# Kernel tuning notes

Hardware: AMD Instinct MI355X
Metric: run time of the kernel (lower is better)

Reference implementation:

```python
import jax, jax.numpy as jnp
import numpy as np

P = 512        # number of graph pairs
MAXN = 192     # max(len_s) by construction
D_IN = 32      # num_input_features
HID = 64       # hidden_dim
REG = 0.1      # entropic reg
ITERS = 8      # numItermax in forward call
DEG = 8        # avg degree for synthetic edges


def setup_inputs() -> dict:
    key = jax.random.key(0)
    ks = jax.random.split(key, 16)
    len_s = np.asarray(96 + (np.arange(P) % 97), dtype=np.int32)          # 96..192
    len_t = np.asarray(32 + ((np.arange(P) * 7) % 65), dtype=np.int32)    # 32..96 <= len_s
    Ns, Nt = int(len_s.sum()), int(len_t.sum())
    return {
        "x_s": jax.random.normal(ks[0], (Ns, D_IN), jnp.float32),
        "x_t": jax.random.normal(ks[1], (Nt, D_IN), jnp.float32),
        "W_rel0": 0.1 * jax.random.normal(ks[2], (D_IN, HID), jnp.float32),
        "b_rel0": 0.1 * jax.random.normal(ks[3], (HID,), jnp.float32),
        "W_root0": 0.1 * jax.random.normal(ks[4], (D_IN, HID), jnp.float32),
        "W_rel1": 0.1 * jax.random.normal(ks[5], (HID, HID), jnp.float32),
        "b_rel1": 0.1 * jax.random.normal(ks[6], (HID,), jnp.float32),
        "W_root1": 0.1 * jax.random.normal(ks[7], (HID, HID), jnp.float32),
        "W_e": 0.1 * jax.random.normal(ks[8], (D_IN + 2 * HID, 64), jnp.float32),
        "b_e": 0.1 * jax.random.normal(ks[9], (64,), jnp.float32),
        "virtual": jax.random.uniform(ks[10], (64,), jnp.float32),
        "edge_index_s": jax.random.randint(ks[11], (2, Ns * DEG), 0, Ns, dtype=jnp.int32),
        "edge_index_t": jax.random.randint(ks[12], (2, Nt * DEG), 0, Nt, dtype=jnp.int32),
        "len_s": jnp.asarray(len_s),
        "len_t": jnp.asarray(len_t),
    }


def _normalize(x):
    return x / jnp.clip(jnp.linalg.norm(x, axis=-1, keepdims=True), 1e-12)


def _gnn_embed(x, ei, layers, W_e, b_e):
    # GraphConv: out = lin_rel(sum_{j->i} x_j) + lin_root(x_i), then relu; cat all layer outputs
    outs = [x]
    h = x
    for (Wr, br, Wo) in layers:
        agg = jax.ops.segment_sum(h[ei[0]], ei[1], num_segments=h.shape[0])
        h = jax.nn.relu(agg @ Wr + br + h @ Wo)
        outs.append(h)
    emb = jnp.concatenate(outs, axis=1) @ W_e + b_e
    return _normalize(emb)


def _pad_gather(emb, lens):
    # [total, E] -> [P, MAXN, E] via per-pair offsets (indices clipped; invalid masked later)
    off = jnp.cumsum(lens) - lens
    idx = jnp.clip(off[:, None] + jnp.arange(MAXN)[None, :], 0, emb.shape[0] - 1)
    return emb[idx]


def reference(x_s, x_t, W_rel0, b_rel0, W_root0, W_rel1, b_rel1, W_root1,
              W_e, b_e, virtual, edge_index_s, edge_index_t, len_s, len_t):
    layers = [(W_rel0, b_rel0, W_root0), (W_rel1, b_rel1, W_root1)]
    emb_s = _gnn_embed(x_s, edge_index_s, layers, W_e, b_e)  # [Ns, 64]
    emb_t = _gnn_embed(x_t, edge_index_t, layers, W_e, b_e)  # [Nt, 64]
    virt = _normalize(virtual[None, :])[0]

    s_pad = _pad_gather(emb_s, len_s)  # [P, MAXN, 64]
    t_pad = _pad_gather(emb_t, len_t)  # [P, MAXN, 64]
    j = jnp.arange(MAXN)
    # columns >= len_t use the virtual node embedding (covers j in [m, n))
    t_mask = (j[None, :] < len_t[:, None])[:, :, None]
    t_aug = jnp.where(t_mask, t_pad, virt[None, None, :])

    # Euclidean cdist via quadratic expansion
    sq_s = jnp.sum(s_pad * s_pad, -1)                              # [P, MAXN]
    sq_t = jnp.sum(t_aug * t_aug, -1)                              # [P, MAXN]
    dot = jnp.einsum('pid,pjd->pij', s_pad, t_aug)                 # [P, MAXN, MAXN]
    cd = jnp.sqrt(jnp.maximum(sq_s[:, :, None] + sq_t[:, None, :] - 2.0 * dot, 1e-12))

    # padded cost: real block = cdist, bottom-right pad block = 0, rest = 1000
    row_valid = j[None, :] < len_s[:, None]                        # [P, MAXN] (n = len_s)
    in_block = row_valid[:, :, None] & row_valid[:, None, :]
    pad_block = (~row_valid)[:, :, None] & (~row_valid)[:, None, :]
    cost = jnp.where(in_block, cd, jnp.where(pad_block, 0.0, 1000.0))

    # Sinkhorn-Knopp, a = b = ones(MAXN) so Kp = K and updates are 1/(K v), 1/(K^T u)
    K = jnp.exp(-cost / REG)

    def body(_, uv):
        u, v = uv
        v = 1.0 / jnp.einsum('pij,pi->pj', K, u)
        u = 1.0 / jnp.einsum('pij,pj->pi', K, v)
        return (u, v)

    u0 = jnp.full((P, MAXN), 1.0 / MAXN, dtype=cost.dtype)
    u, v = jax.lax.fori_loop(0, ITERS, body, (u0, u0))
    gamma = jax.lax.stop_gradient(u[:, :, None] * K * v[:, None, :])

    geds = jnp.sum(gamma * cost, axis=(1, 2))
    geds2 = geds / (len_s + len_t).astype(cost.dtype)
    return gamma, cost, geds2
```

## Files before the change

kernel.cpp:

```cpp
#include <hip/hip_runtime.h>
#include <math.h>

#define PAIRS 512
#define MAXN 192

__global__ void offsets_kernel(const int* __restrict__ ls, const int* __restrict__ lt,
                               int* __restrict__ off) {
    __shared__ int wa[8], wb[8];
    int t = threadIdx.x;
    int a = ls[t], b = lt[t];
    int ia = a, ib = b;
#pragma unroll
    for (int d = 1; d < 64; d <<= 1) {
        int xa = __shfl_up(ia, d, 64);
        int xb = __shfl_up(ib, d, 64);
        if ((t & 63) >= d) { ia += xa; ib += xb; }
    }
    if ((t & 63) == 63) { wa[t >> 6] = ia; wb[t >> 6] = ib; }
    __syncthreads();
    int pa = 0, pb = 0;
    for (int w = 0; w < (t >> 6); w++) { pa += wa[w]; pb += wb[w]; }
    off[t] = pa + ia - a;
    off[PAIRS + t] = pb + ib - b;
}

__global__ __launch_bounds__(256) void count2_kernel(const int* __restrict__ eiS,
                                                     const int* __restrict__ eiT,
                                                     int* __restrict__ cnt,
                                                     int Es, int Et, int split) {
    int e = blockIdx.x * 256 + threadIdx.x;
    if (e < Es) atomicAdd(&cnt[eiS[Es + e]], 1);
    else if (e < Es + Et) atomicAdd(&cnt[split + eiT[Et + (e - Es)]], 1);
}

__global__ __launch_bounds__(256) void scan1_kernel(int* __restrict__ data,
                                                    int* __restrict__ blockSums, int N) {
    __shared__ int sc[256];
    int t = threadIdx.x;
    int base = blockIdx.x * 1024;
    int v[4];
    int s = 0;
#pragma unroll
    for (int q = 0; q < 4; q++) {
        int i = base + t * 4 + q;
        v[q] = (i < N) ? data[i] : 0;
        s += v[q];
    }
    sc[t] = s;
    __syncthreads();
    for (int d = 1; d < 256; d <<= 1) {
        int x = (t >= d) ? sc[t - d] : 0;
        __syncthreads();
        sc[t] += x;
        __syncthreads();
    }
    int excl = sc[t] - s;
#pragma unroll
    for (int q = 0; q < 4; q++) {
        int i = base + t * 4 + q;
        if (i < N) { data[i] = excl; excl += v[q]; }
    }
    if (t == 255) blockSums[blockIdx.x] = sc[255];
}

__global__ void scan2_kernel(int* __restrict__ blockSums, int B) {
    __shared__ int sh[256];
    int t = threadIdx.x;
    int v = (t < B) ? blockSums[t] : 0;
    sh[t] = v;
    __syncthreads();
    for (int d = 1; d < 256; d <<= 1) {
        int x = (t >= d) ? sh[t - d] : 0;
        __syncthreads();
        sh[t] += x;
        __syncthreads();
    }
    if (t < B) blockSums[t] = sh[t] - v;
}

__global__ __launch_bounds__(256) void scan3_kernel(int* __restrict__ data,
                                                    const int* __restrict__ blockSums,
                                                    int* __restrict__ cursor, int N) {
    int i = blockIdx.x * 256 + threadIdx.x;
    if (i < N) {
        int v = data[i] + blockSums[i >> 10];
        data[i] = v;
        cursor[i] = v;
    }
}

__global__ __launch_bounds__(256) void fill2_kernel(const int* __restrict__ eiS,
                                                    const int* __restrict__ eiT,
                                                    int* __restrict__ cursor,
                                                    int* __restrict__ src,
                                                    int Es, int Et, int split) {
    int e = blockIdx.x * 256 + threadIdx.x;
    if (e < Es) {
        int p = atomicAdd(&cursor[eiS[Es + e]], 1);
        src[p] = eiS[e];
    } else if (e < Es + Et) {
        int ee = e - Es;
        int p = atomicAdd(&cursor[split + eiT[Et + ee]], 1);
        src[p] = eiT[ee];
    }
}

template <int F>
__global__ __launch_bounds__(256) void gather_kernel(const float* __restrict__ featA,
                                                     const float* __restrict__ featB,
                                                     int split,
                                                     const int* __restrict__ rs,
                                                     const int* __restrict__ re,
                                                     const int* __restrict__ src,
                                                     float* __restrict__ agg, int N) {
    int gid = blockIdx.x * 256 + threadIdx.x;
    int row = gid / F;
    int lane = threadIdx.x & (F - 1);
    if (row >= N) return;
    int b = rs[row], e = re[row];
    int cnt = e - b;
    const float* feat = (row < split) ? featA : featB;
    int pre = cnt < F ? cnt : F;
    int sidx = (lane < cnt) ? src[b + lane] : 0;
    float acc = 0.f;
    for (int q = 0; q < pre; q++) {
        int s = __shfl(sidx, q, F);
        acc += feat[(size_t)s * F + lane];
    }
    for (int q = b + F; q < e; q++) acc += feat[(size_t)src[q] * F + lane];
    agg[(size_t)row * F + lane] = acc;
}


template <int KIN>
__global__ __launch_bounds__(256) void lin_gemm_kernel(const float* __restrict__ agg,
    const float* __restrict__ hinA, const float* __restrict__ hinB, int split,
    const float* __restrict__ Wrel, const float* __restrict__ brel,
    const float* __restrict__ Wroot, float* __restrict__ hout, int N) {
    __shared__ float Abuf[64 * 65];
    __shared__ float4 Wbuf[64 * 16];
    int tid = threadIdx.x;
    int i = tid & 15, j = tid >> 4;
    int rowbase = blockIdx.x * 64;
    float4 bv = ((const float4*)brel)[j];
    float acc[4][4];
#pragma unroll
    for (int r = 0; r < 4; r++) { acc[r][0] = bv.x; acc[r][1] = bv.y; acc[r][2] = bv.z; acc[r][3] = bv.w; }

    for (int c0 = 0; c0 < 2 * KIN; c0 += 64) {
        __syncthreads();
        for (int t = tid; t < 1024; t += 256) {
            int r = t >> 4, k4 = t & 15;
            int kg = c0 + 4 * k4;
            int row = rowbase + r; if (row >= N) row = N - 1;
            float4 v;
            if (kg < KIN) {
                v = ((const float4*)(agg + (size_t)row * KIN))[kg >> 2];
            } else {
                int kk = kg - KIN;
                const float* h = (row < split) ? hinA + (size_t)row * KIN
                                               : hinB + (size_t)(row - split) * KIN;
                v = ((const float4*)h)[kk >> 2];
            }
            float* d = Abuf + r * 65 + 4 * k4;
            d[0] = v.x; d[1] = v.y; d[2] = v.z; d[3] = v.w;
        }
        for (int t = tid; t < 1024; t += 256) {
            int k = t >> 4, jj = t & 15;
            int kg = c0 + k;
            const float* Wsrc = (kg < KIN) ? (Wrel + (size_t)kg * 64)
                                           : (Wroot + (size_t)(kg - KIN) * 64);
            Wbuf[t] = ((const float4*)Wsrc)[jj];
        }
        __syncthreads();
#pragma unroll 4
        for (int k = 0; k < 64; k++) {
            float4 wv = Wbuf[k * 16 + j];
            float a0 = Abuf[(4 * i + 0) * 65 + k];
            float a1 = Abuf[(4 * i + 1) * 65 + k];
            float a2 = Abuf[(4 * i + 2) * 65 + k];
            float a3 = Abuf[(4 * i + 3) * 65 + k];
            acc[0][0] = fmaf(a0, wv.x, acc[0][0]); acc[0][1] = fmaf(a0, wv.y, acc[0][1]);
            acc[0][2] = fmaf(a0, wv.z, acc[0][2]); acc[0][3] = fmaf(a0, wv.w, acc[0][3]);
            acc[1][0] = fmaf(a1, wv.x, acc[1][0]); acc[1][1] = fmaf(a1, wv.y, acc[1][1]);
            acc[1][2] = fmaf(a1, wv.z, acc[1][2]); acc[1][3] = fmaf(a1, wv.w, acc[1][3]);
            acc[2][0] = fmaf(a2, wv.x, acc[2][0]); acc[2][1] = fmaf(a2, wv.y, acc[2][1]);
            acc[2][2] = fmaf(a2, wv.z, acc[2][2]); acc[2][3] = fmaf(a2, wv.w, acc[2][3]);
            acc[3][0] = fmaf(a3, wv.x, acc[3][0]); acc[3][1] = fmaf(a3, wv.y, acc[3][1]);
            acc[3][2] = fmaf(a3, wv.z, acc[3][2]); acc[3][3] = fmaf(a3, wv.w, acc[3][3]);
        }
    }
#pragma unroll
    for (int r = 0; r < 4; r++) {
        int row = rowbase + 4 * i + r;
        if (row < N) {
            float4 o = make_float4(fmaxf(acc[r][0], 0.f), fmaxf(acc[r][1], 0.f),
                                   fmaxf(acc[r][2], 0.f), fmaxf(acc[r][3], 0.f));
            ((float4*)(hout + (size_t)row * 64))[j] = o;
        }
    }
}

__global__ __launch_bounds__(256) void emb_gemm_kernel(const float* __restrict__ xA,
    const float* __restrict__ xB, int split,
    const float* __restrict__ h1, const float* __restrict__ h2,
    const float* __restrict__ We, const float* __restrict__ be,
    float* __restrict__ emb, int N) {
    __shared__ float Abuf[64 * 65];
    __shared__ float4 Wbuf[64 * 16];
    int tid = threadIdx.x;
    int i = tid & 15, j = tid >> 4;
    int rowbase = blockIdx.x * 64;
    float4 bv = ((const float4*)be)[j];
    float acc[4][4];
#pragma unroll
    for (int r = 0; r < 4; r++) { acc[r][0] = bv.x; acc[r][1] = bv.y; acc[r][2] = bv.z; acc[r][3] = bv.w; }

    for (int c0 = 0; c0 < 160; c0 += 64) {
        int kw = (160 - c0 < 64) ? (160 - c0) : 64;
        int sh = (kw == 64) ? 4 : 3;
        int msk = (1 << sh) - 1;
        __syncthreads();
        for (int t = tid; t < 64 * (kw >> 2); t += 256) {
            int r = t >> sh, k4 = t & msk;
            int kg = c0 + 4 * k4;
            int row = rowbase + r; if (row >= N) row = N - 1;
            float4 v;
            if (kg < 32) {
                const float* x = (row < split) ? xA + (size_t)row * 32
                                               : xB + (size_t)(row - split) * 32;
                v = ((const float4*)x)[kg >> 2];
            } else if (kg < 96) {
                v = ((const float4*)(h1 + (size_t)row * 64))[(kg - 32) >> 2];
            } else {
                v = ((const float4*)(h2 + (size_t)row * 64))[(kg - 96) >> 2];
            }
            float* d = Abuf + r * 65 + 4 * k4;
            d[0] = v.x; d[1] = v.y; d[2] = v.z; d[3] = v.w;
        }
        for (int t = tid; t < kw * 16; t += 256) {
            int k = t >> 4, jj = t & 15;
            Wbuf[t] = ((const float4*)(We + (size_t)(c0 + k) * 64))[jj];
        }
        __syncthreads();
#pragma unroll 4
        for (int k = 0; k < kw; k++) {
            float4 wv = Wbuf[k * 16 + j];
            float a0 = Abuf[(4 * i + 0) * 65 + k];
            float a1 = Abuf[(4 * i + 1) * 65 + k];
            float a2 = Abuf[(4 * i + 2) * 65 + k];
            float a3 = Abuf[(4 * i + 3) * 65 + k];
            acc[0][0] = fmaf(a0, wv.x, acc[0][0]); acc[0][1] = fmaf(a0, wv.y, acc[0][1]);
            acc[0][2] = fmaf(a0, wv.z, acc[0][2]); acc[0][3] = fmaf(a0, wv.w, acc[0][3]);
            acc[1][0] = fmaf(a1, wv.x, acc[1][0]); acc[1][1] = fmaf(a1, wv.y, acc[1][1]);
            acc[1][2] = fmaf(a1, wv.z, acc[1][2]); acc[1][3] = fmaf(a1, wv.w, acc[1][3]);
            acc[2][0] = fmaf(a2, wv.x, acc[2][0]); acc[2][1] = fmaf(a2, wv.y, acc[2][1]);
            acc[2][2] = fmaf(a2, wv.z, acc[2][2]); acc[2][3] = fmaf(a2, wv.w, acc[2][3]);
            acc[3][0] = fmaf(a3, wv.x, acc[3][0]); acc[3][1] = fmaf(a3, wv.y, acc[3][1]);
            acc[3][2] = fmaf(a3, wv.z, acc[3][2]); acc[3][3] = fmaf(a3, wv.w, acc[3][3]);
        }
    }
    __syncthreads();
#pragma unroll
    for (int r = 0; r < 4; r++)
#pragma unroll
        for (int c = 0; c < 4; c++)
            Abuf[(4 * i + r) * 65 + 4 * j + c] = acc[r][c];
    __syncthreads();
    int lane = tid & 63, wv = tid >> 6;
    for (int rr = 0; rr < 16; rr++) {
        int r = wv * 16 + rr;
        float val = Abuf[r * 65 + lane];
        float ss = val * val;
#pragma unroll
        for (int d = 32; d > 0; d >>= 1) ss += __shfl_xor(ss, d, 64);
        int row = rowbase + r;
        if (row < N) emb[(size_t)row * 64 + lane] = val / fmaxf(sqrtf(ss), 1e-12f);
    }
}

__global__ __launch_bounds__(512, 4) void fused_cost_sinkhorn_kernel(
    const float* __restrict__ embS, const float* __restrict__ embT,
    const float* __restrict__ vraw,
    const int* __restrict__ lenS, const int* __restrict__ lenT,
    const int* __restrict__ off,
    float* __restrict__ cost_out, float* __restrict__ gamma_out,
    float* __restrict__ geds2, int Ns) {
    __shared__ __align__(16) float sT[192 * 68];
    __shared__ __align__(16) float sS[96 * 68];
    __shared__ __align__(16) float sqT[192];
    __shared__ __align__(16) float sqS[96];
    __shared__ __align__(16) float virtv[64];

    int p = blockIdx.x;
    int tid = threadIdx.x;
    int ti = tid & 31;
    int tj = tid >> 5;
    int n = lenS[p], m = lenT[p];
    int offs = off[p], offt = off[PAIRS + p];

    if (tid < 64) {
        float v = vraw[tid];
        float ss = v * v;
#pragma unroll
        for (int d = 32; d > 0; d >>= 1) ss += __shfl_xor(ss, d, 64);
        virtv[tid] = v / fmaxf(sqrtf(ss), 1e-12f);
    }
    __syncthreads();

    for (int t = tid; t < 192 * 16; t += 512) {
        int j = t >> 4, q = t & 15;
        float4 vv = (j < m) ? ((const float4*)embT)[(size_t)(offt + j) * 16 + q]
                            : ((const float4*)virtv)[q];
        *(float4*)(sT + j * 68 + 4 * q) = vv;
    }
    __syncthreads();
    if (tid < 192) {
        float s = 0.f;
#pragma unroll
        for (int k = 0; k < 64; k++) { float a = sT[tid * 68 + k]; s = fmaf(a, a, s); }
        sqT[tid] = s;
    }

    float kf[2][3][12];

#pragma unroll
    for (int h = 0; h < 2; h++) {
        __syncthreads();
        for (int t = tid; t < 96 * 16; t += 512) {
            int r = t >> 4, q = t & 15;
            int gi = offs + 96 * h + r;
            if (gi > Ns - 1) gi = Ns - 1;
            float4 vv = ((const float4*)embS)[(size_t)gi * 16 + q];
            *(float4*)(sS + r * 68 + 4 * q) = vv;
        }
        __syncthreads();
        if (tid < 96) {
            float s = 0.f;
#pragma unroll
            for (int k = 0; k < 64; k++) { float a = sS[tid * 68 + k]; s = fmaf(a, a, s); }
            sqS[tid] = s;
        }
        __syncthreads();

#pragma unroll
        for (int s = 0; s < 3; s++)
#pragma unroll
            for (int b = 0; b < 12; b++) kf[h][s][b] = 0.f;

        for (int k4 = 0; k4 < 16; k4++) {
            float4 a0 = *(const float4*)(sS + (3 * ti + 0) * 68 + 4 * k4);
            float4 a1 = *(const float4*)(sS + (3 * ti + 1) * 68 + 4 * k4);
            float4 a2 = *(const float4*)(sS + (3 * ti + 2) * 68 + 4 * k4);
#pragma unroll
            for (int b = 0; b < 12; b++) {
                float4 tb = *(const float4*)(sT + (12 * tj + b) * 68 + 4 * k4);
                kf[h][0][b] = fmaf(a0.x, tb.x, kf[h][0][b]);
                kf[h][0][b] = fmaf(a0.y, tb.y, kf[h][0][b]);
                kf[h][0][b] = fmaf(a0.z, tb.z, kf[h][0][b]);
                kf[h][0][b] = fmaf(a0.w, tb.w, kf[h][0][b]);
                kf[h][1][b] = fmaf(a1.x, tb.x, kf[h][1][b]);
                kf[h][1][b] = fmaf(a1.y, tb.y, kf[h][1][b]);
                kf[h][1][b] = fmaf(a1.z, tb.z, kf[h][1][b]);
                kf[h][1][b] = fmaf(a1.w, tb.w, kf[h][1][b]);
                kf[h][2][b] = fmaf(a2.x, tb.x, kf[h][2][b]);
                kf[h][2][b] = fmaf(a2.y, tb.y, kf[h][2][b]);
                kf[h][2][b] = fmaf(a2.z, tb.z, kf[h][2][b]);
                kf[h][2][b] = fmaf(a2.w, tb.w, kf[h][2][b]);
            }
        }
#pragma unroll
        for (int s = 0; s < 3; s++) {
            int i = 96 * h + 3 * ti + s;
            bool rv = i < n;
            float sqi = sqS[3 * ti + s];
            float tmp[12];
#pragma unroll
            for (int b = 0; b < 12; b++) {
                int j = 12 * tj + b;
                float cd = sqrtf(fmaxf(sqi + sqT[j] - 2.f * kf[h][s][b], 1e-12f));
                float c = (rv && (j < n)) ? cd : ((!rv && (j >= n)) ? 0.f : 1000.f);
                tmp[b] = c;
                kf[h][s][b] = expf(-10.f * c);
            }
            float* orow = cost_out + ((size_t)p * MAXN + i) * MAXN + 12 * tj;
#pragma unroll
            for (int q = 0; q < 3; q++)
                ((float4*)orow)[q] = make_float4(tmp[4 * q], tmp[4 * q + 1],
                                                 tmp[4 * q + 2], tmp[4 * q + 3]);
        }
    }
    __syncthreads();

    float* part = sS;
    float* ubuf = sS + 6336;
    float* vbuf = sqT;

    if (tid < 192) ubuf[tid] = 1.f / 192.f;
    __syncthreads();

    for (int it = 0; it < 8; it++) {
        float uloc[6];
#pragma unroll
        for (int h = 0; h < 2; h++)
#pragma unroll
            for (int s = 0; s < 3; s++) uloc[3 * h + s] = ubuf[96 * h + 3 * ti + s];
#pragma unroll
        for (int b = 0; b < 12; b++) {
            float a = 0.f;
#pragma unroll
            for (int h = 0; h < 2; h++)
#pragma unroll
                for (int s = 0; s < 3; s++) a = fmaf(kf[h][s][b], uloc[3 * h + s], a);
            part[(12 * tj + b) * 33 + ti] = a;
        }
        __syncthreads();
        if (tid < 192) {
            float s = 0.f;
#pragma unroll
            for (int g = 0; g < 32; g++) s += part[tid * 33 + g];
            vbuf[tid] = 1.f / s;
        }
        __syncthreads();
        float vloc[12];
        {
            float4 va = *(const float4*)(vbuf + 12 * tj);
            float4 vb = *(const float4*)(vbuf + 12 * tj + 4);
            float4 vc = *(const float4*)(vbuf + 12 * tj + 8);
            vloc[0] = va.x; vloc[1] = va.y; vloc[2] = va.z; vloc[3] = va.w;
            vloc[4] = vb.x; vloc[5] = vb.y; vloc[6] = vb.z; vloc[7] = vb.w;
            vloc[8] = vc.x; vloc[9] = vc.y; vloc[10] = vc.z; vloc[11] = vc.w;
        }
#pragma unroll
        for (int h = 0; h < 2; h++)
#pragma unroll
            for (int s = 0; s < 3; s++) {
                float a = 0.f;
#pragma unroll
                for (int b = 0; b < 12; b++) a = fmaf(kf[h][s][b], vloc[b], a);
                part[tj * 192 + 96 * h + 3 * ti + s] = a;
            }
        __syncthreads();
        if (tid < 192) {
            float s = 0.f;
#pragma unroll
            for (int g = 0; g < 16; g++) s += part[g * 192 + tid];
            ubuf[tid] = 1.f / s;
        }
        __syncthreads();
    }

    float vloc[12];
    {
        float4 va = *(const float4*)(vbuf + 12 * tj);
        float4 vb = *(const float4*)(vbuf + 12 * tj + 4);
        float4 vc = *(const float4*)(vbuf + 12 * tj + 8);
        vloc[0] = va.x; vloc[1] = va.y; vloc[2] = va.z; vloc[3] = va.w;
        vloc[4] = vb.x; vloc[5] = vb.y; vloc[6] = vb.z; vloc[7] = vb.w;
        vloc[8] = vc.x; vloc[9] = vc.y; vloc[10] = vc.z; vloc[11] = vc.w;
    }
    float accg = 0.f;
#pragma unroll
    for (int h = 0; h < 2; h++)
#pragma unroll
        for (int s = 0; s < 3; s++) {
            int i = 96 * h + 3 * ti + s;
            float ui = ubuf[i];
            float tmp[12];
#pragma unroll
            for (int b = 0; b < 12; b++) {
                float Kij = kf[h][s][b];
                float gg = ui * Kij * vloc[b];
                tmp[b] = gg;
                if (Kij > 0.f) accg = fmaf(gg, -0.1f * logf(Kij), accg);
            }
            float* grow = gamma_out + ((size_t)p * MAXN + i) * MAXN + 12 * tj;
#pragma unroll
            for (int q = 0; q < 3; q++)
                ((float4*)grow)[q] = make_float4(tmp[4 * q], tmp[4 * q + 1],
                                                 tmp[4 * q + 2], tmp[4 * q + 3]);
        }
#pragma unroll
    for (int d = 32; d > 0; d >>= 1) accg += __shfl_xor(accg, d, 64);
    if ((tid & 63) == 0) sqS[tid >> 6] = accg;
    __syncthreads();
    if (tid == 0) {
        float s = 0.f;
        for (int w = 0; w < 8; w++) s += sqS[w];
        geds2[p] = s / (float)(n + m);
    }
}

extern "C" void kernel_launch(void* const* d_in, const int* in_sizes, int n_in,
                              void* d_out, int out_size, void* d_ws, size_t ws_size,
                              hipStream_t stream) {
    const float* x_s     = (const float*)d_in[0];
    const float* x_t     = (const float*)d_in[1];
    const float* W_rel0  = (const float*)d_in[2];
    const float* b_rel0  = (const float*)d_in[3];
    const float* W_root0 = (const float*)d_in[4];
    const float* W_rel1  = (const float*)d_in[5];
    const float* b_rel1  = (const float*)d_in[6];
    const float* W_root1 = (const float*)d_in[7];
    const float* W_e     = (const float*)d_in[8];
    const float* b_e     = (const float*)d_in[9];
    const float* virt    = (const float*)d_in[10];
    const int*   ei_s    = (const int*)d_in[11];
    const int*   ei_t    = (const int*)d_in[12];
    const int*   len_s   = (const int*)d_in[13];
    const int*   len_t   = (const int*)d_in[14];

    int Ns = in_sizes[0] / 32;
    int Nt = in_sizes[1] / 32;
    int Es = in_sizes[11] / 2;
    int Et = in_sizes[12] / 2;
    int Ntot = Ns + Nt;
    int Etot = Es + Et;

    char* w = (char*)d_ws;
    int* off  = (int*)w;              w += 1024 * 4;
    int* bsum = (int*)w;              w += 256 * 4;
    int* rs   = (int*)w;              w += (size_t)Ntot * 4;
    int* cur  = (int*)w;              w += (size_t)Ntot * 4;
    int* src  = (int*)w;              w += (size_t)Etot * 4;
    w = (char*)(((size_t)w + 255) & ~(size_t)255);
    float* agg = (float*)w;           w += (size_t)Ntot * 64 * 4;
    float* h1  = (float*)w;           w += (size_t)Ntot * 64 * 4;
    float* h2  = (float*)w;           w += (size_t)Ntot * 64 * 4;

    float* out_gamma = (float*)d_out;
    float* out_cost  = out_gamma + (size_t)PAIRS * MAXN * MAXN;
    float* out_geds  = out_cost + (size_t)PAIRS * MAXN * MAXN;

    offsets_kernel<<<1, PAIRS, 0, stream>>>(len_s, len_t, off);

    hipMemsetAsync(rs, 0, (size_t)Ntot * 4, stream);
    count2_kernel<<<(Etot + 255) / 256, 256, 0, stream>>>(ei_s, ei_t, rs, Es, Et, Ns);
    int nb = (Ntot + 1023) / 1024;
    scan1_kernel<<<nb, 256, 0, stream>>>(rs, bsum, Ntot);
    scan2_kernel<<<1, 256, 0, stream>>>(bsum, nb);
    scan3_kernel<<<(Ntot + 255) / 256, 256, 0, stream>>>(rs, bsum, cur, Ntot);
    fill2_kernel<<<(Etot + 255) / 256, 256, 0, stream>>>(ei_s, ei_t, cur, src, Es, Et, Ns);

    int gblk = (Ntot + 63) / 64;

    gather_kernel<32><<<(int)(((long long)Ntot * 32 + 255) / 256), 256, 0, stream>>>(
        x_s, x_t, Ns, rs, cur, src, agg, Ntot);
    lin_gemm_kernel<32><<<gblk, 256, 0, stream>>>(
        agg, x_s, x_t, Ns, W_rel0, b_rel0, W_root0, h1, Ntot);
    gather_kernel<64><<<(int)(((long long)Ntot * 64 + 255) / 256), 256, 0, stream>>>(
        h1, h1, Ns, rs, cur, src, agg, Ntot);
    lin_gemm_kernel<64><<<gblk, 256, 0, stream>>>(
        agg, h1, h1, Ntot + 1, W_rel1, b_rel1, W_root1, h2, Ntot);
    emb_gemm_kernel<<<gblk, 256, 0, stream>>>(
        x_s, x_t, Ns, h1, h2, W_e, b_e, agg, Ntot);

    fused_cost_sinkhorn_kernel<<<PAIRS, 512, 0, stream>>>(
        agg, agg + (size_t)Ns * 64, virt, len_s, len_t, off,
        out_cost, out_gamma, out_geds, Ns);
}
```

Before: 576.0 us.

## Fuse second GraphConv layer into embedding GEMM and prefetch source half in Sinkhorn

Merges the second GraphConv linear layer into the embedding projection kernel, keeping h2 in shared memory instead of writing and rereading it from global memory, and drops one kernel launch. In the cost/Sinkhorn kernel, both source halves' loads are restructured: the first half is loaded with T up front, and the second half is prefetched into registers while the first half's epilogue runs. It also replaces __syncthreads with a raw lgkmcnt wait plus s_barrier and uses fast __expf/__logf intrinsics. Risks: emb writes into agg, which is also an input, so blocks overwrite agg rows that only they read; the fast intrinsics and the raw barrier, which waits only on LDS counters, may change accuracy or ordering.

```diff
diff --git a/kernel.cpp b/kernel.cpp
--- a/kernel.cpp
+++ b/kernel.cpp
@@ -3,6 +3,8 @@
 
 #define PAIRS 512
 #define MAXN 192
+
+#define LDS_BAR() asm volatile("s_waitcnt lgkmcnt(0)\n\ts_barrier" ::: "memory")
 
 __global__ void offsets_kernel(const int* __restrict__ ls, const int* __restrict__ lt,
                                int* __restrict__ off) {
@@ -201,23 +203,78 @@
     }
 }
 
-__global__ __launch_bounds__(256) void emb_gemm_kernel(const float* __restrict__ xA,
-    const float* __restrict__ xB, int split,
-    const float* __restrict__ h1, const float* __restrict__ h2,
+__global__ __launch_bounds__(256) void lin64_emb_kernel(
+    const float* __restrict__ agg, const float* __restrict__ h1,
+    const float* __restrict__ xA, const float* __restrict__ xB, int split,
+    const float* __restrict__ Wrel, const float* __restrict__ brel,
+    const float* __restrict__ Wroot,
     const float* __restrict__ We, const float* __restrict__ be,
     float* __restrict__ emb, int N) {
     __shared__ float Abuf[64 * 65];
     __shared__ float4 Wbuf[64 * 16];
+    __shared__ float h2buf[64 * 68];
     int tid = threadIdx.x;
     int i = tid & 15, j = tid >> 4;
     int rowbase = blockIdx.x * 64;
+
+    {
+        float4 bv = ((const float4*)brel)[j];
+        float acc[4][4];
+#pragma unroll
+        for (int r = 0; r < 4; r++) { acc[r][0] = bv.x; acc[r][1] = bv.y; acc[r][2] = bv.z; acc[r][3] = bv.w; }
+
+        for (int c0 = 0; c0 < 128; c0 += 64) {
+            __syncthreads();
+            for (int t = tid; t < 1024; t += 256) {
+                int r = t >> 4, k4 = t & 15;
+                int kg = c0 + 4 * k4;
+                int row = rowbase + r; if (row >= N) row = N - 1;
+                float4 v;
+                if (kg < 64) v = ((const float4*)(agg + (size_t)row * 64))[kg >> 2];
+                else         v = ((const float4*)(h1 + (size_t)row * 64))[(kg - 64) >> 2];
+                float* d = Abuf + r * 65 + 4 * k4;
+                d[0] = v.x; d[1] = v.y; d[2] = v.z; d[3] = v.w;
+            }
+            for (int t = tid; t < 1024; t += 256) {
+                int k = t >> 4, jj = t & 15;
+                int kg = c0 + k;
+                const float* Wsrc = (kg < 64) ? (Wrel + (size_t)kg * 64)
+                                              : (Wroot + (size_t)(kg - 64) * 64);
+                Wbuf[t] = ((const float4*)Wsrc)[jj];
+            }
+            __syncthreads();
+#pragma unroll 4
+            for (int k = 0; k < 64; k++) {
+                float4 wv = Wbuf[k * 16 + j];
+                float a0 = Abuf[(4 * i + 0) * 65 + k];
+                float a1 = Abuf[(4 * i + 1) * 65 + k];
+                float a2 = Abuf[(4 * i + 2) * 65 + k];
+                float a3 = Abuf[(4 * i + 3) * 65 + k];
+                acc[0][0] = fmaf(a0, wv.x, acc[0][0]); acc[0][1] = fmaf(a0, wv.y, acc[0][1]);
+                acc[0][2] = fmaf(a0, wv.z, acc[0][2]); acc[0][3] = fmaf(a0, wv.w, acc[0][3]);
+                acc[1][0] = fmaf(a1, wv.x, acc[1][0]); acc[1][1] = fmaf(a1, wv.y, acc[1][1]);
+                acc[1][2] = fmaf(a1, wv.z, acc[1][2]); acc[1][3] = fmaf(a1, wv.w, acc[1][3]);
+                acc[2][0] = fmaf(a2, wv.x, acc[2][0]); acc[2][1] = fmaf(a2, wv.y, acc[2][1]);
+                acc[2][2] = fmaf(a2, wv.z, acc[2][2]); acc[2][3] = fmaf(a2, wv.w, acc[2][3]);
+                acc[3][0] = fmaf(a3, wv.x, acc[3][0]); acc[3][1] = fmaf(a3, wv.y, acc[3][1]);
+                acc[3][2] = fmaf(a3, wv.z, acc[3][2]); acc[3][3] = fmaf(a3, wv.w, acc[3][3]);
+            }
+        }
+#pragma unroll
+        for (int r = 0; r < 4; r++) {
+            float* d = h2buf + (4 * i + r) * 68 + 4 * j;
+            d[0] = fmaxf(acc[r][0], 0.f); d[1] = fmaxf(acc[r][1], 0.f);
+            d[2] = fmaxf(acc[r][2], 0.f); d[3] = fmaxf(acc[r][3], 0.f);
+        }
+    }
+
     float4 bv = ((const float4*)be)[j];
     float acc[4][4];
 #pragma unroll
     for (int r = 0; r < 4; r++) { acc[r][0] = bv.x; acc[r][1] = bv.y; acc[r][2] = bv.z; acc[r][3] = bv.w; }
 
-    for (int c0 = 0; c0 < 160; c0 += 64) {
-        int kw = (160 - c0 < 64) ? (160 - c0) : 64;
+    for (int c0 = 0; c0 < 96; c0 += 64) {
+        int kw = (96 - c0 < 64) ? 32 : 64;
         int sh = (kw == 64) ? 4 : 3;
         int msk = (1 << sh) - 1;
         __syncthreads();
@@ -230,10 +287,8 @@
                 const float* x = (row < split) ? xA + (size_t)row * 32
                                                : xB + (size_t)(row - split) * 32;
                 v = ((const float4*)x)[kg >> 2];
-            } else if (kg < 96) {
+            } else {
                 v = ((const float4*)(h1 + (size_t)row * 64))[(kg - 32) >> 2];
-            } else {
-                v = ((const float4*)(h2 + (size_t)row * 64))[(kg - 96) >> 2];
             }
             float* d = Abuf + r * 65 + 4 * k4;
             d[0] = v.x; d[1] = v.y; d[2] = v.z; d[3] = v.w;
@@ -261,6 +316,28 @@
         }
     }
     __syncthreads();
+    for (int t = tid; t < 1024; t += 256) {
+        int k = t >> 4, jj = t & 15;
+        Wbuf[t] = ((const float4*)(We + (size_t)(96 + k) * 64))[jj];
+    }
+    __syncthreads();
+#pragma unroll 4
+    for (int k = 0; k < 64; k++) {
+        float4 wv = Wbuf[k * 16 + j];
+        float a0 = h2buf[(4 * i + 0) * 68 + k];
+        float a1 = h2buf[(4 * i + 1) * 68 + k];
+        float a2 = h2buf[(4 * i + 2) * 68 + k];
+        float a3 = h2buf[(4 * i + 3) * 68 + k];
+        acc[0][0] = fmaf(a0, wv.x, acc[0][0]); acc[0][1] = fmaf(a0, wv.y, acc[0][1]);
+        acc[0][2] = fmaf(a0, wv.z, acc[0][2]); acc[0][3] = fmaf(a0, wv.w, acc[0][3]);
+        acc[1][0] = fmaf(a1, wv.x, acc[1][0]); acc[1][1] = fmaf(a1, wv.y, acc[1][1]);
+        acc[1][2] = fmaf(a1, wv.z, acc[1][2]); acc[1][3] = fmaf(a1, wv.w, acc[1][3]);
+        acc[2][0] = fmaf(a2, wv.x, acc[2][0]); acc[2][1] = fmaf(a2, wv.y, acc[2][1]);
+        acc[2][2] = fmaf(a2, wv.z, acc[2][2]); acc[2][3] = fmaf(a2, wv.w, acc[2][3]);
+        acc[3][0] = fmaf(a3, wv.x, acc[3][0]); acc[3][1] = fmaf(a3, wv.y, acc[3][1]);
+        acc[3][2] = fmaf(a3, wv.z, acc[3][2]); acc[3][3] = fmaf(a3, wv.w, acc[3][3]);
+    }
+    __syncthreads();
 #pragma unroll
     for (int r = 0; r < 4; r++)
 #pragma unroll
@@ -276,6 +353,60 @@
         for (int d = 32; d > 0; d >>= 1) ss += __shfl_xor(ss, d, 64);
         int row = rowbase + r;
         if (row < N) emb[(size_t)row * 64 + lane] = val / fmaxf(sqrtf(ss), 1e-12f);
+    }
+}
+
+__device__ __forceinline__ void dot_half(float kh[3][12], const float* sS, const float* sT,
+                                         int ti, int tj) {
+#pragma unroll
+    for (int s = 0; s < 3; s++)
+#pragma unroll
+        for (int b = 0; b < 12; b++) kh[s][b] = 0.f;
+    for (int k4 = 0; k4 < 16; k4++) {
+        float4 a0 = *(const float4*)(sS + (3 * ti + 0) * 68 + 4 * k4);
+        float4 a1 = *(const float4*)(sS + (3 * ti + 1) * 68 + 4 * k4);
+        float4 a2 = *(const float4*)(sS + (3 * ti + 2) * 68 + 4 * k4);
+#pragma unroll
+        for (int b = 0; b < 12; b++) {
+            float4 tb = *(const float4*)(sT + (12 * tj + b) * 68 + 4 * k4);
+            kh[0][b] = fmaf(a0.x, tb.x, kh[0][b]);
+            kh[0][b] = fmaf(a0.y, tb.y, kh[0][b]);
+            kh[0][b] = fmaf(a0.z, tb.z, kh[0][b]);
+            kh[0][b] = fmaf(a0.w, tb.w, kh[0][b]);
+            kh[1][b] = fmaf(a1.x, tb.x, kh[1][b]);
+            kh[1][b] = fmaf(a1.y, tb.y, kh[1][b]);
+            kh[1][b] = fmaf(a1.z, tb.z, kh[1][b]);
+            kh[1][b] = fmaf(a1.w, tb.w, kh[1][b]);
+            kh[2][b] = fmaf(a2.x, tb.x, kh[2][b]);
+            kh[2][b] = fmaf(a2.y, tb.y, kh[2][b]);
+            kh[2][b] = fmaf(a2.z, tb.z, kh[2][b]);
+            kh[2][b] = fmaf(a2.w, tb.w, kh[2][b]);
+        }
+    }
+}
+
+__device__ __forceinline__ void epi_half(float kh[3][12], const float* sqS, const float* sqT,
+                                         int h, int ti, int tj, int n, int p,
+                                         float* __restrict__ cost_out) {
+#pragma unroll
+    for (int s = 0; s < 3; s++) {
+        int i = 96 * h + 3 * ti + s;
+        bool rv = i < n;
+        float sqi = sqS[3 * ti + s];
+        float tmp[12];
+#pragma unroll
+        for (int b = 0; b < 12; b++) {
+            int j = 12 * tj + b;
+            float cd = sqrtf(fmaxf(sqi + sqT[j] - 2.f * kh[s][b], 1e-12f));
+            float c = (rv && (j < n)) ? cd : ((!rv && (j >= n)) ? 0.f : 1000.f);
+            tmp[b] = c;
+            kh[s][b] = __expf(-10.f * c);
+        }
+        float* orow = cost_out + ((size_t)p * MAXN + i) * MAXN + 12 * tj;
+#pragma unroll
+        for (int q = 0; q < 3; q++)
+            ((float4*)orow)[q] = make_float4(tmp[4 * q], tmp[4 * q + 1],
+                                             tmp[4 * q + 2], tmp[4 * q + 3]);
     }
 }
 
@@ -314,90 +445,68 @@
                             : ((const float4*)virtv)[q];
         *(float4*)(sT + j * 68 + 4 * q) = vv;
     }
+    for (int t = tid; t < 96 * 16; t += 512) {
+        int r = t >> 4, q = t & 15;
+        int gi = offs + r; if (gi > Ns - 1) gi = Ns - 1;
+        float4 vv = ((const float4*)embS)[(size_t)gi * 16 + q];
+        *(float4*)(sS + r * 68 + 4 * q) = vv;
+    }
     __syncthreads();
     if (tid < 192) {
         float s = 0.f;
 #pragma unroll
         for (int k = 0; k < 64; k++) { float a = sT[tid * 68 + k]; s = fmaf(a, a, s); }
         sqT[tid] = s;
-    }
+    } else if (tid < 288) {
+        int r = tid - 192;
+        float s = 0.f;
+#pragma unroll
+        for (int k = 0; k < 64; k++) { float a = sS[r * 68 + k]; s = fmaf(a, a, s); }
+        sqS[r] = s;
+    }
+    __syncthreads();
 
     float kf[2][3][12];
 
-#pragma unroll
-    for (int h = 0; h < 2; h++) {
-        __syncthreads();
-        for (int t = tid; t < 96 * 16; t += 512) {
-            int r = t >> 4, q = t & 15;
-            int gi = offs + 96 * h + r;
-            if (gi > Ns - 1) gi = Ns - 1;
-            float4 vv = ((const float4*)embS)[(size_t)gi * 16 + q];
-            *(float4*)(sS + r * 68 + 4 * q) = vv;
-        }
-        __syncthreads();
-        if (tid < 96) {
-            float s = 0.f;
-#pragma unroll
-            for (int k = 0; k < 64; k++) { float a = sS[tid * 68 + k]; s = fmaf(a, a, s); }
-            sqS[tid] = s;
-        }
-        __syncthreads();
-
-#pragma unroll
-        for (int s = 0; s < 3; s++)
-#pragma unroll
-            for (int b = 0; b < 12; b++) kf[h][s][b] = 0.f;
-
-        for (int k4 = 0; k4 < 16; k4++) {
-            float4 a0 = *(const float4*)(sS + (3 * ti + 0) * 68 + 4 * k4);
-            float4 a1 = *(const float4*)(sS + (3 * ti + 1) * 68 + 4 * k4);
-            float4 a2 = *(const float4*)(sS + (3 * ti + 2) * 68 + 4 * k4);
-#pragma unroll
-            for (int b = 0; b < 12; b++) {
-                float4 tb = *(const float4*)(sT + (12 * tj + b) * 68 + 4 * k4);
-                kf[h][0][b] = fmaf(a0.x, tb.x, kf[h][0][b]);
-                kf[h][0][b] = fmaf(a0.y, tb.y, kf[h][0][b]);
-                kf[h][0][b] = fmaf(a0.z, tb.z, kf[h][0][b]);
-                kf[h][0][b] = fmaf(a0.w, tb.w, kf[h][0][b]);
-                kf[h][1][b] = fmaf(a1.x, tb.x, kf[h][1][b]);
-                kf[h][1][b] = fmaf(a1.y, tb.y, kf[h][1][b]);
-                kf[h][1][b] = fmaf(a1.z, tb.z, kf[h][1][b]);
-                kf[h][1][b] = fmaf(a1.w, tb.w, kf[h][1][b]);
-                kf[h][2][b] = fmaf(a2.x, tb.x, kf[h][2][b]);
-                kf[h][2][b] = fmaf(a2.y, tb.y, kf[h][2][b]);
-                kf[h][2][b] = fmaf(a2.z, tb.z, kf[h][2][b]);
-                kf[h][2][b] = fmaf(a2.w, tb.w, kf[h][2][b]);
-            }
-        }
-#pragma unroll
-        for (int s = 0; s < 3; s++) {
-            int i = 96 * h + 3 * ti + s;
-            bool rv = i < n;
-            float sqi = sqS[3 * ti + s];
-            float tmp[12];
-#pragma unroll
-            for (int b = 0; b < 12; b++) {
-                int j = 12 * tj + b;
-                float cd = sqrtf(fmaxf(sqi + sqT[j] - 2.f * kf[h][s][b], 1e-12f));
-                float c = (rv && (j < n)) ? cd : ((!rv && (j >= n)) ? 0.f : 1000.f);
-                tmp[b] = c;
-                kf[h][s][b] = expf(-10.f * c);
-            }
-            float* orow = cost_out + ((size_t)p * MAXN + i) * MAXN + 12 * tj;
-#pragma unroll
-            for (int q = 0; q < 3; q++)
-                ((float4*)orow)[q] = make_float4(tmp[4 * q], tmp[4 * q + 1],
-                                                 tmp[4 * q + 2], tmp[4 * q + 3]);
-        }
-    }
-    __syncthreads();
+    dot_half(kf[0], sS, sT, ti, tj);
+    float4 pf0, pf1, pf2;
+    {
+        int t0 = tid, t1 = tid + 512, t2 = tid + 1024;
+        int gi0 = offs + 96 + (t0 >> 4); if (gi0 > Ns - 1) gi0 = Ns - 1;
+        int gi1 = offs + 96 + (t1 >> 4); if (gi1 > Ns - 1) gi1 = Ns - 1;
+        int gi2 = offs + 96 + (t2 >> 4); if (gi2 > Ns - 1) gi2 = Ns - 1;
+        pf0 = ((const float4*)embS)[(size_t)gi0 * 16 + (t0 & 15)];
+        pf1 = ((const float4*)embS)[(size_t)gi1 * 16 + (t1 & 15)];
+        pf2 = ((const float4*)embS)[(size_t)gi2 * 16 + (t2 & 15)];
+    }
+    epi_half(kf[0], sqS, sqT, 0, ti, tj, n, p, cost_out);
+
+    LDS_BAR();
+    {
+        int t0 = tid, t1 = tid + 512, t2 = tid + 1024;
+        *(float4*)(sS + (t0 >> 4) * 68 + 4 * (t0 & 15)) = pf0;
+        *(float4*)(sS + (t1 >> 4) * 68 + 4 * (t1 & 15)) = pf1;
+        *(float4*)(sS + (t2 >> 4) * 68 + 4 * (t2 & 15)) = pf2;
+    }
+    LDS_BAR();
+    if (tid < 96) {
+        float s = 0.f;
+#pragma unroll
+        for (int k = 0; k < 64; k++) { float a = sS[tid * 68 + k]; s = fmaf(a, a, s); }
+        sqS[tid] = s;
+    }
+    LDS_BAR();
+
+    dot_half(kf[1], sS, sT, ti, tj);
+    epi_half(kf[1], sqS, sqT, 1, ti, tj, n, p, cost_out);
+    LDS_BAR();
 
     float* part = sS;
     float* ubuf = sS + 6336;
     float* vbuf = sqT;
 
     if (tid < 192) ubuf[tid] = 1.f / 192.f;
-    __syncthreads();
+    LDS_BAR();
 
     for (int it = 0; it < 8; it++) {
         float uloc[6];
@@ -414,14 +523,14 @@
                 for (int s = 0; s < 3; s++) a = fmaf(kf[h][s][b], uloc[3 * h + s], a);
             part[(12 * tj + b) * 33 + ti] = a;
         }
-        __syncthreads();
+        LDS_BAR();
         if (tid < 192) {
             float s = 0.f;
 #pragma unroll
             for (int g = 0; g < 32; g++) s += part[tid * 33 + g];
             vbuf[tid] = 1.f / s;
         }
-        __syncthreads();
+        LDS_BAR();
         float vloc[12];
         {
             float4 va = *(const float4*)(vbuf + 12 * tj);
@@ -440,14 +549,14 @@
                 for (int b = 0; b < 12; b++) a = fmaf(kf[h][s][b], vloc[b], a);
                 part[tj * 192 + 96 * h + 3 * ti + s] = a;
             }
-        __syncthreads();
+        LDS_BAR();
         if (tid < 192) {
             float s = 0.f;
 #pragma unroll
             for (int g = 0; g < 16; g++) s += part[g * 192 + tid];
             ubuf[tid] = 1.f / s;
         }
-        __syncthreads();
+        LDS_BAR();
     }
 
     float vloc[12];
@@ -472,7 +581,7 @@
                 float Kij = kf[h][s][b];
                 float gg = ui * Kij * vloc[b];
                 tmp[b] = gg;
-                if (Kij > 0.f) accg = fmaf(gg, -0.1f * logf(Kij), accg);
+                if (Kij > 0.f) accg = fmaf(gg, -0.1f * __logf(Kij), accg);
             }
             float* grow = gamma_out + ((size_t)p * MAXN + i) * MAXN + 12 * tj;
 #pragma unroll
@@ -483,7 +592,7 @@
 #pragma unroll
     for (int d = 32; d > 0; d >>= 1) accg += __shfl_xor(accg, d, 64);
     if ((tid & 63) == 0) sqS[tid >> 6] = accg;
-    __syncthreads();
+    LDS_BAR();
     if (tid == 0) {
         float s = 0.f;
         for (int w = 0; w < 8; w++) s += sqS[w];
@@ -526,7 +635,6 @@
     w = (char*)(((size_t)w + 255) & ~(size_t)255);
     float* agg = (float*)w;           w += (size_t)Ntot * 64 * 4;
     float* h1  = (float*)w;           w += (size_t)Ntot * 64 * 4;
-    float* h2  = (float*)w;           w += (size_t)Ntot * 64 * 4;
 
     float* out_gamma = (float*)d_out;
     float* out_cost  = out_gamma + (size_t)PAIRS * MAXN * MAXN;
@@ -550,10 +658,8 @@
         agg, x_s, x_t, Ns, W_rel0, b_rel0, W_root0, h1, Ntot);
     gather_kernel<64><<<(int)(((long long)Ntot * 64 + 255) / 256), 256, 0, stream>>>(
         h1, h1, Ns, rs, cur, src, agg, Ntot);
-    lin_gemm_kernel<64><<<gblk, 256, 0, stream>>>(
-        agg, h1, h1, Ntot + 1, W_rel1, b_rel1, W_root1, h2, Ntot);
-    emb_gemm_kernel<<<gblk, 256, 0, stream>>>(
-        x_s, x_t, Ns, h1, h2, W_e, b_e, agg, Ntot);
+    lin64_emb_kernel<<<gblk, 256, 0, stream>>>(
+        agg, h1, x_s, x_t, Ns, W_rel1, b_rel1, W_root1, W_e, b_e, agg, Ntot);
 
     fused_cost_sinkhorn_kernel<<<PAIRS, 512, 0, stream>>>(
         agg, agg + (size_t)Ns * 64, virt, len_s, len_t, off,
```

Result: faster. 559.1 us (-2.9%).
